# Performance work log

Measured on AMD Instinct MI355X. Metric: run time of the kernel, lower is better.

The kernel has to match this reference:

```python
import jax, jax.numpy as jnp
import numpy as np

B, T, HID = 2, 1024, 4096
H, D_NOPE, D_ROPE, D_V = 32, 128, 64, 128
D_QK = D_NOPE + D_ROPE  # 192
Q_RANK, KV_RANK = 1536, 512
THETA, EPS = 10000.0, 1e-6
SCALE = D_QK ** -0.5
NEG = -1e30


def rms_norm(x, w):
    return x * jax.lax.rsqrt(jnp.mean(x * x, axis=-1, keepdims=True) + EPS) * w


def apply_rope(x, positions):
    # x: [B, T, h, d] (d even), positions: [B, T]
    d = x.shape[-1]
    inv_freq = 1.0 / (THETA ** (jnp.arange(0, d, 2, dtype=jnp.float32) / d))
    ang = positions.astype(jnp.float32)[:, :, None, None] * inv_freq  # [B,T,1,d/2]
    cos, sin = jnp.cos(ang), jnp.sin(ang)
    x1, x2 = jnp.split(x, 2, axis=-1)
    return jnp.concatenate([x1 * cos - x2 * sin, x1 * sin + x2 * cos], axis=-1)


def setup_inputs() -> dict:
    key = jax.random.key(0)
    ks = jax.random.split(key, 8)
    def lin(k, fan_in, fan_out):
        return (jax.random.normal(k, (fan_in, fan_out), jnp.float32)
                / np.float32(np.sqrt(fan_in)))
    return {
        "x": jax.random.normal(ks[0], (B, T, HID), jnp.float32),
        "wq_a": lin(ks[1], HID, Q_RANK),
        "q_norm_w": jnp.ones((Q_RANK,), jnp.float32),
        "wq_b": lin(ks[2], Q_RANK, H * D_QK),
        "wkv_a": lin(ks[3], HID, KV_RANK + D_ROPE),
        "kv_norm_w": jnp.ones((KV_RANK,), jnp.float32),
        "wkv_b": lin(ks[4], KV_RANK, H * (D_NOPE + D_V)),
        "wo": lin(ks[5], H * D_V, HID),
        "attention_mask": jnp.ones((B, T), jnp.int32),
        "positions": jnp.broadcast_to(jnp.arange(T, dtype=jnp.int32), (B, T)),
    }


def reference(x, wq_a, q_norm_w, wq_b, wkv_a, kv_norm_w, wkv_b, wo,
              attention_mask, positions):
    # ---- query path: low-rank down-proj, RMSNorm, up-proj ----
    q = rms_norm(x @ wq_a, q_norm_w) @ wq_b           # [B,T,H*D_QK]
    q = q.reshape(B, T, H, D_QK)
    q_nope, q_pe = jnp.split(q, [D_NOPE], axis=-1)
    q_pe = apply_rope(q_pe, positions)                # [B,T,H,D_ROPE]

    # ---- kv path: compressed latent + shared rope key ----
    kv_out = x @ wkv_a                                # [B,T,KV_RANK+D_ROPE]
    kv, k_pe = jnp.split(kv_out, [KV_RANK], axis=-1)
    k_pe = apply_rope(k_pe[:, :, None, :], positions) # [B,T,1,D_ROPE]
    kv_exp = rms_norm(kv, kv_norm_w) @ wkv_b          # [B,T,H*(D_NOPE+D_V)]
    kv_exp = kv_exp.reshape(B, T, H, D_NOPE + D_V)
    k_nope, v = jnp.split(kv_exp, [D_NOPE], axis=-1)

    q = jnp.concatenate([q_nope, q_pe], axis=-1)      # [B,T,H,D_QK]
    k = jnp.concatenate(
        [k_nope, jnp.broadcast_to(k_pe, (B, T, H, D_ROPE))], axis=-1)

    # ---- attention (causal + padding mask) ----
    scores = jnp.einsum('bthd,bshd->bhts', q, k) * SCALE     # [B,H,T,T]
    causal = jnp.tril(jnp.ones((T, T), dtype=bool))
    mask = causal[None, None] & (attention_mask[:, None, None, :] != 0)
    scores = jnp.where(mask, scores, NEG)
    attn = jax.nn.softmax(scores, axis=-1)
    out = jnp.einsum('bhts,bshd->bthd', attn, v)              # [B,T,H,D_V]
    return out.reshape(B, T, H * D_V) @ wo                    # [B,T,HID]
```

## Files before the change

kernel.cpp:

```cpp
#include <hip/hip_runtime.h>
#include <hip/hip_bf16.h>

#define BB 2
#define TT 1024
#define HIDD 4096
#define NH 32
#define DN 128
#define DR 64
#define DVV 128
#define DQK 192
#define QR 1536
#define KVR 512
#define MTOK (BB*TT)
#define EPSF 1e-6f
#define SCALEF 0.07216878364870322f

typedef unsigned short u16;
using bfrag = __attribute__((ext_vector_type(8))) short;
using f4 = __attribute__((ext_vector_type(4))) float;

__device__ __forceinline__ float bf2f(u16 u){
    union { unsigned int i; float f; } v; v.i = ((unsigned int)u) << 16; return v.f;
}
__device__ __forceinline__ u16 f2bf(float f){
    union { float f; unsigned int i; } v; v.f = f;
    unsigned int r = v.i + 0x7fffu + ((v.i >> 16) & 1u);
    return (u16)(r >> 16);
}
__device__ __forceinline__ void async16(const void* g, void* l){
    __builtin_amdgcn_global_load_lds((const __attribute__((address_space(1))) void*)g,
                                     (__attribute__((address_space(3))) void*)l, 16, 0, 0);
}

__global__ __launch_bounds__(256) void cvt_k(const float* __restrict__ in,
                                             u16* __restrict__ out, int n)
{
    int i = (blockIdx.x * 256 + threadIdx.x) * 4;
    if (i >= n) return;
    float4 v = *(const float4*)(in + i);
    ushort4 o = make_ushort4(f2bf(v.x), f2bf(v.y), f2bf(v.z), f2bf(v.w));
    *(ushort4*)(out + i) = o;
}

__global__ __launch_bounds__(256) void transpose_cvt(
    const float* __restrict__ W, u16* __restrict__ Wt, int Kd, int Nd)
{
    __shared__ u16 S[32][33];
    const int n0 = blockIdx.x * 32, k0 = blockIdx.y * 32;
    const int tx = threadIdx.x & 31, ty = threadIdx.x >> 5;
    #pragma unroll
    for (int i = 0; i < 4; ++i)
        S[ty + 8 * i][tx] = f2bf(W[(size_t)(k0 + ty + 8 * i) * Nd + n0 + tx]);
    __syncthreads();
    #pragma unroll
    for (int i = 0; i < 4; ++i)
        Wt[(size_t)(n0 + ty + 8 * i) * Kd + k0 + tx] = S[tx][ty + 8 * i];
}

template<int BN, int CMODE>
__global__ __launch_bounds__(256) void gemm_bt(
    const u16* __restrict__ A, const u16* __restrict__ Bt, void* __restrict__ C,
    u16* __restrict__ C2, int M, int N, int K, int lda)
{
    constexpr int BM = 128, BK = 32;
    constexpr int WAVES_N = (BN == 128) ? 2 : 1;
    constexpr int WAVES_M = 4 / WAVES_N;
    constexpr int WM = BM / WAVES_M, WN = BN / WAVES_N;
    constexpr int FM = WM / 16, FN = WN / 16;
    constexpr int RPWB = BN / 4;
    __shared__ alignas(16) u16 As[BM * BK];
    __shared__ alignas(16) u16 Bs[BN * BK];
    const int tid = threadIdx.x, w = tid >> 6, ln = tid & 63;
    const int row0 = blockIdx.y * BM, col0 = blockIdx.x * BN;
    const int wm = w / WAVES_N, wn = w % WAVES_N;
    const int lr = ln & 15, lq = ln >> 4;

    f4 acc[FM][FN];
    #pragma unroll
    for (int i = 0; i < FM; ++i)
        #pragma unroll
        for (int j = 0; j < FN; ++j)
            acc[i][j] = (f4){0.f, 0.f, 0.f, 0.f};

    const u16* gA = A + (size_t)(row0 + w * 32 + (ln >> 2)) * lda + (ln & 3) * 8;
    const u16* gB = Bt + (size_t)(col0 + w * RPWB + (ln >> 2)) * K + (ln & 3) * 8;

    for (int k0 = 0; k0 < K; k0 += BK) {
        #pragma unroll
        for (int i = 0; i < 2; ++i)
            async16(gA + (size_t)i * 16 * lda + k0, &As[(w * 32 + i * 16) * BK]);
        #pragma unroll
        for (int i = 0; i < RPWB / 16; ++i)
            async16(gB + (size_t)i * 16 * K + k0, &Bs[(w * RPWB + i * 16) * BK]);
        __syncthreads();
        bfrag af[FM], bf[FN];
        #pragma unroll
        for (int fm = 0; fm < FM; ++fm)
            af[fm] = *(const bfrag*)&As[(wm * WM + fm * 16 + lr) * BK + lq * 8];
        #pragma unroll
        for (int fn = 0; fn < FN; ++fn)
            bf[fn] = *(const bfrag*)&Bs[(wn * WN + fn * 16 + lr) * BK + lq * 8];
        #pragma unroll
        for (int fm = 0; fm < FM; ++fm)
            #pragma unroll
            for (int fn = 0; fn < FN; ++fn)
                acc[fm][fn] = __builtin_amdgcn_mfma_f32_16x16x32_bf16(
                    af[fm], bf[fn], acc[fm][fn], 0, 0, 0);
        __syncthreads();
    }
    #pragma unroll
    for (int fm = 0; fm < FM; ++fm)
        #pragma unroll
        for (int fn = 0; fn < FN; ++fn) {
            const int col = col0 + wn * WN + fn * 16 + lr;
            const int rowb = row0 + wm * WM + fm * 16 + lq * 4;
            if (CMODE == 2) {
                const int head = col >> 8, within = col & 255;
                if (within < DN) {
                    #pragma unroll
                    for (int r = 0; r < 4; ++r)
                        ((u16*)C)[(size_t)(rowb + r) * (NH * DN) + head * DN + within]
                            = f2bf(acc[fm][fn][r]);
                } else {
                    ushort4 pk = make_ushort4(f2bf(acc[fm][fn][0]), f2bf(acc[fm][fn][1]),
                                              f2bf(acc[fm][fn][2]), f2bf(acc[fm][fn][3]));
                    size_t off = ((size_t)((rowb >> 10) * NH + head) * DVV + (within - DN)) * TT
                                 + (rowb & (TT - 1));
                    *(ushort4*)(C2 + off) = pk;
                }
            } else {
                #pragma unroll
                for (int r = 0; r < 4; ++r) {
                    size_t off = (size_t)(rowb + r) * N + col;
                    if (CMODE == 1) ((float*)C)[off] = acc[fm][fn][r];
                    else            ((u16*)C)[off] = f2bf(acc[fm][fn][r]);
                }
            }
        }
}

__global__ __launch_bounds__(256) void rmsnorm_bf(
    u16* __restrict__ p, const float* __restrict__ w, int W, int stride)
{
    u16* x = p + (size_t)blockIdx.x * stride;
    __shared__ float red[256];
    float s = 0.f;
    for (int c = threadIdx.x; c < W; c += 256) { float v = bf2f(x[c]); s += v * v; }
    red[threadIdx.x] = s;
    __syncthreads();
    for (int off = 128; off > 0; off >>= 1) {
        if (threadIdx.x < off) red[threadIdx.x] += red[threadIdx.x + off];
        __syncthreads();
    }
    float scale = rsqrtf(red[0] / (float)W + EPSF);
    for (int c = threadIdx.x; c < W; c += 256)
        x[c] = f2bf(bf2f(x[c]) * scale * w[c]);
}

__global__ void rope_q_k(u16* __restrict__ q, const int* __restrict__ pos)
{
    int idx = blockIdx.x * 256 + threadIdx.x;
    if (idx >= MTOK * NH * 32) return;
    int j = idx & 31, h = (idx >> 5) & 31, tok = idx >> 10;
    u16* p = q + (size_t)tok * (NH * DQK) + h * DQK + DN;
    float x1 = bf2f(p[j]), x2 = bf2f(p[j + 32]);
    float inv = powf(10000.0f, -(float)j / 32.0f);
    float ang = (float)pos[tok] * inv;
    float sn, cs; sincosf(ang, &sn, &cs);
    p[j] = f2bf(x1 * cs - x2 * sn);
    p[j + 32] = f2bf(x1 * sn + x2 * cs);
}

__global__ void rope_k_k(const u16* __restrict__ kvd, u16* __restrict__ kpe,
                         const int* __restrict__ pos)
{
    int idx = blockIdx.x * 256 + threadIdx.x;
    if (idx >= MTOK * 32) return;
    int j = idx & 31, tok = idx >> 5;
    const u16* p = kvd + (size_t)tok * 576 + KVR;
    float x1 = bf2f(p[j]), x2 = bf2f(p[j + 32]);
    float inv = powf(10000.0f, -(float)j / 32.0f);
    float ang = (float)pos[tok] * inv;
    float sn, cs; sincosf(ang, &sn, &cs);
    kpe[(size_t)tok * 64 + j] = f2bf(x1 * cs - x2 * sn);
    kpe[(size_t)tok * 64 + j + 32] = f2bf(x1 * sn + x2 * cs);
}

struct SMa {
    alignas(16) u16 Ks[64 * 200];
    alignas(16) u16 Ps[4][16 * 72];
    float Msk[64];
};
struct SMb { alignas(16) u16 Ot[64 * 136]; };
union SMu { SMa a; SMb o; };

__global__ __launch_bounds__(256) void attn_mfma(
    const u16* __restrict__ q, const u16* __restrict__ KN,
    const u16* __restrict__ kpe, const u16* __restrict__ VT,
    const int* __restrict__ amask, u16* __restrict__ O)
{
    __shared__ SMu sm;
    const int tid = threadIdx.x, w = tid >> 6, ln = tid & 63;
    const int lr = ln & 15, lq = ln >> 4;
    const int h = blockIdx.y, b = blockIdx.z;
    const u16* vtb = VT + (size_t)(b * NH + h) * DVV * TT;

    #pragma unroll
    for (int pass = 0; pass < 2; ++pass) {
        const int t = pass ? (15 - blockIdx.x) : blockIdx.x;
        const int q0 = t * 64;
        const int qg0 = q0 + w * 16 + lq * 4;

        bfrag qf[6];
        const u16* qbase = q + (size_t)(b * TT + q0 + w * 16 + lr) * (NH * DQK) + h * DQK + lq * 8;
        #pragma unroll
        for (int ks = 0; ks < 6; ++ks) qf[ks] = *(const bfrag*)(qbase + ks * 32);

        f4 acc[8];
        #pragma unroll
        for (int i = 0; i < 8; ++i) acc[i] = (f4){0.f, 0.f, 0.f, 0.f};
        float m_i[4], l_i[4];
        #pragma unroll
        for (int r = 0; r < 4; ++r) { m_i[r] = -1e30f; l_i[r] = 0.f; }

        const int nkt = t + 1;
        for (int kt = 0; kt < nkt; ++kt) {
            const int k0 = kt * 64;
            __syncthreads();
            #pragma unroll
            for (int it = 0; it < 12; ++it) {
                int u = it * 256 + tid;
                int row = u / 48, col = (u % 48) * 4;
                ushort4 kv4;
                if (col < DN)
                    kv4 = *(const ushort4*)&KN[(size_t)(b * TT + k0 + row) * (NH * DN) + h * DN + col];
                else
                    kv4 = *(const ushort4*)&kpe[(size_t)(b * TT + k0 + row) * 64 + (col - DN)];
                *(ushort4*)&sm.a.Ks[row * 200 + col] = kv4;
            }
            if (tid < 64) sm.a.Msk[tid] = amask[b * TT + k0 + tid] ? 0.f : -1e30f;
            __syncthreads();

            f4 sacc[4];
            #pragma unroll
            for (int nt = 0; nt < 4; ++nt) {
                sacc[nt] = (f4){0.f, 0.f, 0.f, 0.f};
                #pragma unroll
                for (int ks = 0; ks < 6; ++ks) {
                    bfrag kf = *(const bfrag*)&sm.a.Ks[(nt * 16 + lr) * 200 + ks * 32 + lq * 8];
                    sacc[nt] = __builtin_amdgcn_mfma_f32_16x16x32_bf16(qf[ks], kf, sacc[nt], 0, 0, 0);
                }
            }
            float mb[4]; int keyg[4];
            #pragma unroll
            for (int nt = 0; nt < 4; ++nt) {
                keyg[nt] = k0 + nt * 16 + lr;
                mb[nt] = sm.a.Msk[nt * 16 + lr];
            }
            float s[4][4];
            #pragma unroll
            for (int nt = 0; nt < 4; ++nt)
                #pragma unroll
                for (int r = 0; r < 4; ++r) {
                    float v = sacc[nt][r] * SCALEF + mb[nt];
                    s[nt][r] = (keyg[nt] <= qg0 + r) ? v : -1e30f;
                }
            #pragma unroll
            for (int r = 0; r < 4; ++r) {
                float tm = fmaxf(fmaxf(s[0][r], s[1][r]), fmaxf(s[2][r], s[3][r]));
                tm = fmaxf(tm, __shfl_xor(tm, 1));
                tm = fmaxf(tm, __shfl_xor(tm, 2));
                tm = fmaxf(tm, __shfl_xor(tm, 4));
                tm = fmaxf(tm, __shfl_xor(tm, 8));
                float m_new = fmaxf(m_i[r], tm);
                float alpha = __expf(m_i[r] - m_new);
                float p0 = __expf(s[0][r] - m_new);
                float p1 = __expf(s[1][r] - m_new);
                float p2 = __expf(s[2][r] - m_new);
                float p3 = __expf(s[3][r] - m_new);
                float rs = (p0 + p1) + (p2 + p3);
                rs += __shfl_xor(rs, 1);
                rs += __shfl_xor(rs, 2);
                rs += __shfl_xor(rs, 4);
                rs += __shfl_xor(rs, 8);
                l_i[r] = l_i[r] * alpha + rs;
                m_i[r] = m_new;
                #pragma unroll
                for (int d = 0; d < 8; ++d) acc[d][r] *= alpha;
                sm.a.Ps[w][(lq * 4 + r) * 72 + lr] = f2bf(p0);
                sm.a.Ps[w][(lq * 4 + r) * 72 + 16 + lr] = f2bf(p1);
                sm.a.Ps[w][(lq * 4 + r) * 72 + 32 + lr] = f2bf(p2);
                sm.a.Ps[w][(lq * 4 + r) * 72 + 48 + lr] = f2bf(p3);
            }
            bfrag pf0 = *(const bfrag*)&sm.a.Ps[w][lr * 72 + lq * 8];
            bfrag pf1 = *(const bfrag*)&sm.a.Ps[w][lr * 72 + 32 + lq * 8];
            #pragma unroll
            for (int d = 0; d < 8; ++d) {
                bfrag vf0 = *(const bfrag*)(vtb + (size_t)(d * 16 + lr) * TT + k0 + lq * 8);
                bfrag vf1 = *(const bfrag*)(vtb + (size_t)(d * 16 + lr) * TT + k0 + 32 + lq * 8);
                acc[d] = __builtin_amdgcn_mfma_f32_16x16x32_bf16(pf0, vf0, acc[d], 0, 0, 0);
                acc[d] = __builtin_amdgcn_mfma_f32_16x16x32_bf16(pf1, vf1, acc[d], 0, 0, 0);
            }
        }
        float inv_l[4];
        #pragma unroll
        for (int r = 0; r < 4; ++r) inv_l[r] = 1.0f / l_i[r];
        __syncthreads();
        #pragma unroll
        for (int d = 0; d < 8; ++d)
            #pragma unroll
            for (int r = 0; r < 4; ++r)
                sm.o.Ot[(w * 16 + lq * 4 + r) * 136 + d * 16 + lr] = f2bf(acc[d][r] * inv_l[r]);
        __syncthreads();
        #pragma unroll
        for (int it = 0; it < 8; ++it) {
            int u = it * 256 + tid;
            int orow = u >> 5, ocol = (u & 31) * 4;
            ushort4 o4 = *(const ushort4*)&sm.o.Ot[orow * 136 + ocol];
            *(ushort4*)&O[(size_t)(b * TT + q0 + orow) * (NH * DVV) + h * DVV + ocol] = o4;
        }
    }
}

extern "C" void kernel_launch(void* const* d_in, const int* in_sizes, int n_in,
                              void* d_out, int out_size, void* d_ws, size_t ws_size,
                              hipStream_t stream)
{
    const float* x      = (const float*)d_in[0];
    const float* wq_a   = (const float*)d_in[1];
    const float* q_nw   = (const float*)d_in[2];
    const float* wq_b   = (const float*)d_in[3];
    const float* wkv_a  = (const float*)d_in[4];
    const float* kv_nw  = (const float*)d_in[5];
    const float* wkv_b  = (const float*)d_in[6];
    const float* wo     = (const float*)d_in[7];
    const int* amask    = (const int*)d_in[8];
    const int* pos      = (const int*)d_in[9];

    u16* ws = (u16*)d_ws;
    u16* wqa_t  = ws;
    u16* wqb_t  = wqa_t  + (size_t)QR * HIDD;
    u16* wkva_t = wqb_t  + (size_t)NH * DQK * QR;
    u16* wkvb_t = wkva_t + (size_t)576 * HIDD;
    u16* wo_t   = wkvb_t + (size_t)NH * 256 * KVR;
    u16* xb     = wo_t   + (size_t)HIDD * HIDD;
    u16* q_down = xb     + (size_t)MTOK * HIDD;
    u16* qbuf   = q_down + (size_t)MTOK * QR;
    u16* kvd    = qbuf   + (size_t)MTOK * NH * DQK;
    u16* kpe    = kvd    + (size_t)MTOK * 576;
    u16* KN     = kpe    + (size_t)MTOK * 64;
    u16* VT     = KN     + (size_t)MTOK * NH * DN;
    u16* Obuf   = wqa_t;

    cvt_k<<<(MTOK*HIDD/4 + 255)/256, 256, 0, stream>>>(x, xb, MTOK*HIDD);
    transpose_cvt<<<dim3(QR/32, HIDD/32), 256, 0, stream>>>(wq_a, wqa_t, HIDD, QR);
    transpose_cvt<<<dim3(NH*DQK/32, QR/32), 256, 0, stream>>>(wq_b, wqb_t, QR, NH*DQK);
    transpose_cvt<<<dim3(576/32, HIDD/32), 256, 0, stream>>>(wkv_a, wkva_t, HIDD, 576);
    transpose_cvt<<<dim3(NH*256/32, KVR/32), 256, 0, stream>>>(wkv_b, wkvb_t, KVR, NH*256);
    transpose_cvt<<<dim3(HIDD/32, HIDD/32), 256, 0, stream>>>(wo, wo_t, HIDD, HIDD);

    gemm_bt<128, 0><<<dim3(QR/128, MTOK/128), 256, 0, stream>>>(
        xb, wqa_t, q_down, nullptr, MTOK, QR, HIDD, HIDD);
    gemm_bt<64, 0><<<dim3(576/64, MTOK/128), 256, 0, stream>>>(
        xb, wkva_t, kvd, nullptr, MTOK, 576, HIDD, HIDD);
    rmsnorm_bf<<<MTOK, 256, 0, stream>>>(q_down, q_nw, QR, QR);
    rmsnorm_bf<<<MTOK, 256, 0, stream>>>(kvd, kv_nw, KVR, 576);
    rope_k_k<<<(MTOK*32 + 255)/256, 256, 0, stream>>>(kvd, kpe, pos);
    gemm_bt<128, 0><<<dim3(NH*DQK/128, MTOK/128), 256, 0, stream>>>(
        q_down, wqb_t, qbuf, nullptr, MTOK, NH*DQK, QR, QR);
    gemm_bt<128, 2><<<dim3(NH*256/128, MTOK/128), 256, 0, stream>>>(
        kvd, wkvb_t, KN, VT, MTOK, NH*256, KVR, 576);
    rope_q_k<<<(MTOK*NH*32 + 255)/256, 256, 0, stream>>>(qbuf, pos);
    attn_mfma<<<dim3(8, NH, BB), 256, 0, stream>>>(qbuf, KN, kpe, VT, amask, Obuf);
    gemm_bt<128, 1><<<dim3(HIDD/128, MTOK/128), 256, 0, stream>>>(
        Obuf, wo_t, (float*)d_out, nullptr, MTOK, HIDD, NH*DVV, NH*DVV);
}
```

Measured before the change: 705.7 us.

## Double-buffer swizzled K tiles with async loads and prefetch V in attention

```diff
diff --git a/kernel.cpp b/kernel.cpp
--- a/kernel.cpp
+++ b/kernel.cpp
@@ -164,7 +164,7 @@
     int j = idx & 31, h = (idx >> 5) & 31, tok = idx >> 10;
     u16* p = q + (size_t)tok * (NH * DQK) + h * DQK + DN;
     float x1 = bf2f(p[j]), x2 = bf2f(p[j + 32]);
-    float inv = powf(10000.0f, -(float)j / 32.0f);
+    float inv = __expf((float)j * -0.28782313662425572f);
     float ang = (float)pos[tok] * inv;
     float sn, cs; sincosf(ang, &sn, &cs);
     p[j] = f2bf(x1 * cs - x2 * sn);
@@ -179,7 +179,7 @@
     int j = idx & 31, tok = idx >> 5;
     const u16* p = kvd + (size_t)tok * 576 + KVR;
     float x1 = bf2f(p[j]), x2 = bf2f(p[j + 32]);
-    float inv = powf(10000.0f, -(float)j / 32.0f);
+    float inv = __expf((float)j * -0.28782313662425572f);
     float ang = (float)pos[tok] * inv;
     float sn, cs; sincosf(ang, &sn, &cs);
     kpe[(size_t)tok * 64 + j] = f2bf(x1 * cs - x2 * sn);
@@ -187,14 +187,13 @@
 }
 
 struct SMa {
-    alignas(16) u16 Ks[64 * 200];
+    alignas(16) u16 Ks[2][64 * 192];
     alignas(16) u16 Ps[4][16 * 72];
-    float Msk[64];
 };
 struct SMb { alignas(16) u16 Ot[64 * 136]; };
 union SMu { SMa a; SMb o; };
 
-__global__ __launch_bounds__(256) void attn_mfma(
+__global__ __launch_bounds__(256, 2) void attn_mfma(
     const u16* __restrict__ q, const u16* __restrict__ KN,
     const u16* __restrict__ kpe, const u16* __restrict__ VT,
     const int* __restrict__ amask, u16* __restrict__ O)
@@ -202,12 +201,26 @@
     __shared__ SMu sm;
     const int tid = threadIdx.x, w = tid >> 6, ln = tid & 63;
     const int lr = ln & 15, lq = ln >> 4;
-    const int h = blockIdx.y, b = blockIdx.z;
+    const int h = blockIdx.x, b = blockIdx.z;
     const u16* vtb = VT + (size_t)(b * NH + h) * DVV * TT;
 
+    auto stage = [&](u16* dst, int k0) {
+        #pragma unroll
+        for (int i = 0; i < 6; ++i) {
+            const int p = (w * 6 + i) * 64 + ln;
+            const int row = p / 24;
+            const int c = (p - row * 24) ^ (row & 7);
+            const int col = c << 3;
+            const u16* src = (col < DN)
+                ? KN + (size_t)(b * TT + k0 + row) * (NH * DN) + h * DN + col
+                : kpe + (size_t)(b * TT + k0 + row) * 64 + (col - DN);
+            async16(src, dst + (w * 6 + i) * 512);
+        }
+    };
+
     #pragma unroll
     for (int pass = 0; pass < 2; ++pass) {
-        const int t = pass ? (15 - blockIdx.x) : blockIdx.x;
+        const int t = pass ? (15 - blockIdx.y) : blockIdx.y;
         const int q0 = t * 64;
         const int qg0 = q0 + w * 16 + lq * 4;
 
@@ -223,48 +236,53 @@
         #pragma unroll
         for (int r = 0; r < 4; ++r) { m_i[r] = -1e30f; l_i[r] = 0.f; }
 
+        __syncthreads();
+        stage(sm.a.Ks[0], 0);
+        __syncthreads();
+
+        u16* cur = sm.a.Ks[0];
+        u16* nxt = sm.a.Ks[1];
         const int nkt = t + 1;
         for (int kt = 0; kt < nkt; ++kt) {
             const int k0 = kt * 64;
-            __syncthreads();
-            #pragma unroll
-            for (int it = 0; it < 12; ++it) {
-                int u = it * 256 + tid;
-                int row = u / 48, col = (u % 48) * 4;
-                ushort4 kv4;
-                if (col < DN)
-                    kv4 = *(const ushort4*)&KN[(size_t)(b * TT + k0 + row) * (NH * DN) + h * DN + col];
-                else
-                    kv4 = *(const ushort4*)&kpe[(size_t)(b * TT + k0 + row) * 64 + (col - DN)];
-                *(ushort4*)&sm.a.Ks[row * 200 + col] = kv4;
-            }
-            if (tid < 64) sm.a.Msk[tid] = amask[b * TT + k0 + tid] ? 0.f : -1e30f;
-            __syncthreads();
+
+            float mb[4];
+            #pragma unroll
+            for (int nt = 0; nt < 4; ++nt)
+                mb[nt] = amask[b * TT + k0 + nt * 16 + lr] ? 0.f : -1e30f;
+            bfrag vf0[8], vf1[8];
+            #pragma unroll
+            for (int d = 0; d < 8; ++d) {
+                const u16* vrow = vtb + (size_t)(d * 16 + lr) * TT + k0 + lq * 8;
+                vf0[d] = *(const bfrag*)vrow;
+                vf1[d] = *(const bfrag*)(vrow + 32);
+            }
+            if (kt + 1 < nkt) stage(nxt, k0 + 64);
 
             f4 sacc[4];
             #pragma unroll
             for (int nt = 0; nt < 4; ++nt) {
                 sacc[nt] = (f4){0.f, 0.f, 0.f, 0.f};
+                const int r_ = nt * 16 + lr;
+                const u16* kr = cur + r_ * 192;
+                const int sw = r_ & 7;
                 #pragma unroll
                 for (int ks = 0; ks < 6; ++ks) {
-                    bfrag kf = *(const bfrag*)&sm.a.Ks[(nt * 16 + lr) * 200 + ks * 32 + lq * 8];
+                    bfrag kf = *(const bfrag*)(kr + (((ks * 4 + lq) ^ sw) << 3));
                     sacc[nt] = __builtin_amdgcn_mfma_f32_16x16x32_bf16(qf[ks], kf, sacc[nt], 0, 0, 0);
                 }
             }
-            float mb[4]; int keyg[4];
+
+            float s[4][4];
             #pragma unroll
             for (int nt = 0; nt < 4; ++nt) {
-                keyg[nt] = k0 + nt * 16 + lr;
-                mb[nt] = sm.a.Msk[nt * 16 + lr];
-            }
-            float s[4][4];
-            #pragma unroll
-            for (int nt = 0; nt < 4; ++nt)
+                const int keyg = k0 + nt * 16 + lr;
                 #pragma unroll
                 for (int r = 0; r < 4; ++r) {
                     float v = sacc[nt][r] * SCALEF + mb[nt];
-                    s[nt][r] = (keyg[nt] <= qg0 + r) ? v : -1e30f;
+                    s[nt][r] = (keyg <= qg0 + r) ? v : -1e30f;
                 }
+            }
             #pragma unroll
             for (int r = 0; r < 4; ++r) {
                 float tm = fmaxf(fmaxf(s[0][r], s[1][r]), fmaxf(s[2][r], s[3][r]));
@@ -296,16 +314,15 @@
             bfrag pf1 = *(const bfrag*)&sm.a.Ps[w][lr * 72 + 32 + lq * 8];
             #pragma unroll
             for (int d = 0; d < 8; ++d) {
-                bfrag vf0 = *(const bfrag*)(vtb + (size_t)(d * 16 + lr) * TT + k0 + lq * 8);
-                bfrag vf1 = *(const bfrag*)(vtb + (size_t)(d * 16 + lr) * TT + k0 + 32 + lq * 8);
-                acc[d] = __builtin_amdgcn_mfma_f32_16x16x32_bf16(pf0, vf0, acc[d], 0, 0, 0);
-                acc[d] = __builtin_amdgcn_mfma_f32_16x16x32_bf16(pf1, vf1, acc[d], 0, 0, 0);
-            }
+                acc[d] = __builtin_amdgcn_mfma_f32_16x16x32_bf16(pf0, vf0[d], acc[d], 0, 0, 0);
+                acc[d] = __builtin_amdgcn_mfma_f32_16x16x32_bf16(pf1, vf1[d], acc[d], 0, 0, 0);
+            }
+            __syncthreads();
+            u16* tmp = cur; cur = nxt; nxt = tmp;
         }
         float inv_l[4];
         #pragma unroll
         for (int r = 0; r < 4; ++r) inv_l[r] = 1.0f / l_i[r];
-        __syncthreads();
         #pragma unroll
         for (int d = 0; d < 8; ++d)
             #pragma unroll
@@ -371,7 +388,7 @@
     gemm_bt<128, 2><<<dim3(NH*256/128, MTOK/128), 256, 0, stream>>>(
         kvd, wkvb_t, KN, VT, MTOK, NH*256, KVR, 576);
     rope_q_k<<<(MTOK*NH*32 + 255)/256, 256, 0, stream>>>(qbuf, pos);
-    attn_mfma<<<dim3(8, NH, BB), 256, 0, stream>>>(qbuf, KN, kpe, VT, amask, Obuf);
+    attn_mfma<<<dim3(NH, 8, BB), 256, 0, stream>>>(qbuf, KN, kpe, VT, amask, Obuf);
     gemm_bt<128, 1><<<dim3(HIDD/128, MTOK/128), 256, 0, stream>>>(
         Obuf, wo_t, (float*)d_out, nullptr, MTOK, HIDD, NH*DVV, NH*DVV);
 }
```

Result: faster. 658.9 us (-6.6%).
